# Performance work log

Hardware: AMD Instinct MI355X
Metric: run time of the kernel (lower is better)

The kernel has to match this reference:

```python
import jax, jax.numpy as jnp
import numpy as np

EPS = 1e-6

def _layernorm(x, gamma, beta):
    mu = jnp.mean(x, axis=-1, keepdims=True)
    var = jnp.mean(jnp.square(x - mu), axis=-1, keepdims=True)
    return (x - mu) * jax.lax.rsqrt(var + EPS) * gamma + beta


def setup_inputs() -> dict:
    key = jax.random.key(0)
    ks = jax.random.split(key, 8)
    B, N, C, F = 2, 2048, 1024, 4096
    s = 0.02
    return {
        "x": jax.random.normal(ks[0], (B, N, C), jnp.float32),
        "Wq": jax.random.normal(ks[1], (C, C), jnp.float32) * s,
        "Wk": jax.random.normal(ks[2], (C, C), jnp.float32) * s,
        "Wv": jax.random.normal(ks[3], (C, C), jnp.float32) * s,
        "Wp": jax.random.normal(ks[4], (C, C), jnp.float32) * s,
        "bp": jnp.zeros((C,), jnp.float32),
        "W1": jax.random.normal(ks[5], (C, F), jnp.float32) * s,
        "b1": jnp.zeros((F,), jnp.float32),
        "W2": jax.random.normal(ks[6], (F, C), jnp.float32) * s,
        "b2": jnp.zeros((C,), jnp.float32),
        "gamma1": jnp.ones((C,), jnp.float32),
        "beta1": jnp.zeros((C,), jnp.float32),
        "gamma2": jnp.ones((C,), jnp.float32),
        "beta2": jnp.zeros((C,), jnp.float32),
    }


def reference(x, Wq, Wk, Wv, Wp, bp, W1, b1, W2, b2, gamma1, beta1, gamma2, beta2):
    B, N, C = x.shape
    H = 16
    D = C // H
    scale = D ** -0.5

    xn = _layernorm(x, gamma1, beta1)
    # QKV projections (no bias); q pre-scaled by head_dim**-0.5 as in source
    q = (xn @ Wq * scale).reshape(B, N, H, D).transpose(0, 2, 1, 3)  # bhnd
    k = (xn @ Wk).reshape(B, N, H, D).transpose(0, 2, 1, 3)
    v = (xn @ Wv).reshape(B, N, H, D).transpose(0, 2, 1, 3)

    attn = jax.nn.softmax(jnp.einsum("bhnd,bhmd->bhnm", q, k), axis=-1)
    y = jnp.einsum("bhnm,bhmd->bhnd", attn, v)
    y = y.transpose(0, 2, 1, 3).reshape(B, N, C)
    x = x + (y @ Wp + bp)

    xn2 = _layernorm(x, gamma2, beta2)
    h = jax.nn.gelu(xn2 @ W1 + b1, approximate=False)  # keras 'gelu' is exact
    x = x + (h @ W2 + b2)
    return x
```

## Files before the change

kernel.cpp:

```cpp
#include <hip/hip_runtime.h>
#include <math.h>

#define BN  4096
#define SEQ 2048
#define CH  1024
#define FF  4096
#define NH  16
#define HD  64

typedef short bf16x8 __attribute__((ext_vector_type(8)));
typedef float f32x4  __attribute__((ext_vector_type(4)));

#define MFMA16(a,b,c) __builtin_amdgcn_mfma_f32_16x16x32_bf16(a,b,c,0,0,0)

__device__ __forceinline__ unsigned short f2b(float f){
  unsigned u = __float_as_uint(f);
  u += 0x7fffu + ((u>>16)&1u);
  return (unsigned short)(u>>16);
}

__device__ __forceinline__ unsigned pk2(float a, float b){
  return __builtin_amdgcn_perm(__float_as_uint(b), __float_as_uint(a), 0x07060302u);
}

#if __has_builtin(__builtin_amdgcn_exp2f)
__device__ __forceinline__ float fexp2(float x){ return __builtin_amdgcn_exp2f(x); }
#else
__device__ __forceinline__ float fexp2(float x){
  float r; asm("v_exp_f32 %0, %1" : "=v"(r) : "v"(x)); return r;
}
#endif

__device__ __forceinline__ void gl2lds16(const void* g, void* l){
  __builtin_amdgcn_global_load_lds(
      (__attribute__((address_space(1))) void*)g,
      (__attribute__((address_space(3))) void*)l, 16, 0, 0);
}

__device__ __forceinline__ unsigned xcd_chunk(unsigned id, unsigned nwg){
  const unsigned cpx = nwg >> 3;
  return (id & 7u)*cpx + (id >> 3);
}

__global__ __launch_bounds__(256) void transpose_cvt(const float* __restrict__ in,
    unsigned short* __restrict__ out, int R, int S, float scale)
{
  __shared__ float tile[64][65];
  const int tid = threadIdx.x;
  const int tx = tid & 63, ty = tid >> 6;
  const int s0 = blockIdx.x * 64, r0 = blockIdx.y * 64;
  #pragma unroll
  for (int j = 0; j < 16; j++){
    int r = ty + j*4;
    tile[r][tx] = in[(size_t)(r0 + r)*S + s0 + tx];
  }
  __syncthreads();
  #pragma unroll
  for (int j = 0; j < 16; j++){
    int s = ty + j*4;
    out[(size_t)(s0 + s)*R + r0 + tx] = f2b(tile[tx][s] * scale);
  }
}

__global__ __launch_bounds__(256) void ln_kernel(const float* __restrict__ x,
    const float* __restrict__ gamma, const float* __restrict__ beta,
    unsigned short* __restrict__ out)
{
  const int row = blockIdx.x, tid = threadIdx.x;
  const float4 xv = ((const float4*)(x + (size_t)row*CH))[tid];
  float s  = xv.x + xv.y + xv.z + xv.w;
  float ss = xv.x*xv.x + xv.y*xv.y + xv.z*xv.z + xv.w*xv.w;
  #pragma unroll
  for (int off = 1; off < 64; off <<= 1){
    s  += __shfl_xor(s,  off, 64);
    ss += __shfl_xor(ss, off, 64);
  }
  __shared__ float red[8];
  const int w = tid >> 6;
  if ((tid & 63) == 0){ red[w] = s; red[4+w] = ss; }
  __syncthreads();
  s  = red[0]+red[1]+red[2]+red[3];
  ss = red[4]+red[5]+red[6]+red[7];
  const float mu   = s * (1.f/CH);
  const float rstd = rsqrtf(ss*(1.f/CH) - mu*mu + 1e-6f);
  const float4 g = ((const float4*)gamma)[tid];
  const float4 b = ((const float4*)beta )[tid];
  ushort4 o;
  o.x = f2b((xv.x-mu)*rstd*g.x + b.x);
  o.y = f2b((xv.y-mu)*rstd*g.y + b.y);
  o.z = f2b((xv.z-mu)*rstd*g.z + b.z);
  o.w = f2b((xv.w-mu)*rstd*g.w + b.w);
  ((ushort4*)(out + (size_t)row*CH))[tid] = o;
}

template<int BNT,int BIAS,int GELU,int RES,int OMODE,int SPLITK>
__global__ __launch_bounds__(256,2) void gemm_bt(const unsigned short* __restrict__ A,
    const unsigned short* __restrict__ Bt, const float* __restrict__ bias,
    const float* __restrict__ resid, float* __restrict__ outF,
    unsigned short* __restrict__ outB, unsigned short* __restrict__ outK,
    unsigned short* __restrict__ outV, int M, int Nn, int K)
{
  constexpr int MI  = (BNT==128) ? 4 : 2;
  constexpr int BCH = (BNT==128) ? 4 : 2;
  constexpr int ABYTES = 128*64*2;
  constexpr int BBYTES = BNT*64*2;
  __shared__ __align__(16) char lds[2*ABYTES + 2*BBYTES];
  const int tid = threadIdx.x;
  const int w = tid >> 6, lane = tid & 63;
  const int quad = lane >> 4, l16 = lane & 15;
  const unsigned Wid = xcd_chunk(blockIdx.y*gridDim.x + blockIdx.x,
                                 gridDim.x*gridDim.y);
  const int bx = Wid % gridDim.x, by = Wid / gridDim.x;
  const int m0 = by*128, n0 = bx*BNT;
  const int wm = (BNT==128) ? (w >> 1)*64 : w*32;
  const int wn = (BNT==128) ? (w & 1)*64 : 0;
  const int srow = lane >> 3, sslot = lane & 7;
  f32x4 acc[MI][4] = {};
  const int kseg = SPLITK > 1 ? K / SPLITK : K;
  const int kBeg = SPLITK > 1 ? blockIdx.z * kseg : 0;
  const int nsteps = kseg >> 6;

  auto STAGE = [&](int buf, int k0){
    char* Ad = lds + buf*ABYTES;
    char* Bd = lds + 2*ABYTES + buf*BBYTES;
    #pragma unroll
    for (int i = 0; i < 4; i++){
      const int rb = (w*4 + i)*8;
      const int r = rb + srow;
      const int c = sslot ^ (r & 7);
      gl2lds16(A + (size_t)(m0 + r)*K + k0 + c*8, Ad + rb*128);
    }
    #pragma unroll
    for (int i = 0; i < BCH; i++){
      const int rb = (w*BCH + i)*8;
      const int r = rb + srow;
      const int c = sslot ^ (r & 7);
      gl2lds16(Bt + (size_t)(n0 + r)*K + k0 + c*8, Bd + rb*128);
    }
  };

  STAGE(0, kBeg);
  __syncthreads();
  for (int t = 0; t < nsteps; t++){
    const int cur = t & 1;
    if (t + 1 < nsteps) STAGE(cur ^ 1, kBeg + (t+1)*64);
    const unsigned short* Ac = (const unsigned short*)(lds + cur*ABYTES);
    const unsigned short* Bc = (const unsigned short*)(lds + 2*ABYTES + cur*BBYTES);
    #pragma unroll
    for (int kc = 0; kc < 2; kc++){
      bf16x8 af[MI], bfr[4];
      #pragma unroll
      for (int mi = 0; mi < MI; mi++){
        const int r = wm + mi*16 + l16;
        af[mi] = *(const bf16x8*)(Ac + r*64 + (((kc*4 + quad) ^ (r & 7))*8));
      }
      #pragma unroll
      for (int nj = 0; nj < 4; nj++){
        const int r = wn + nj*16 + l16;
        bfr[nj] = *(const bf16x8*)(Bc + r*64 + (((kc*4 + quad) ^ (r & 7))*8));
      }
      #pragma unroll
      for (int mi = 0; mi < MI; mi++)
        #pragma unroll
        for (int nj = 0; nj < 4; nj++)
          acc[mi][nj] = MFMA16(af[mi], bfr[nj], acc[mi][nj]);
    }
    __syncthreads();
  }

  if (OMODE == 1 || OMODE == 3){
    unsigned short* scr = (unsigned short*)lds + w*(64*64);
    #pragma unroll
    for (int nj = 0; nj < 4; nj++){
      const int col = n0 + wn + nj*16 + l16;
      const float bv = BIAS ? bias[col] : 0.f;
      #pragma unroll
      for (int mi = 0; mi < MI; mi++){
        #pragma unroll
        for (int r = 0; r < 4; r++){
          const int rl = mi*16 + quad*4 + r;
          float v = acc[mi][nj][r] + bv;
          if (GELU) v = 0.5f*v*(1.f + erff(v*0.70710678118654752f));
          if (RES)  v += resid[(size_t)(m0 + wm + rl)*Nn + col];
          const unsigned short b16 = f2b(v);
          if (OMODE == 3 && (n0 + wn) >= 2048){
            const int d = nj*16 + l16;
            scr[d*64 + (((rl & 15) << 2) | (rl >> 4))] = b16;
          } else {
            scr[rl*64 + nj*16 + l16] = b16;
          }
        }
      }
    }
    const int row0 = m0 + wm;
    const int colb = n0 + wn;
    const int sl = (lane & 7)*8;
    #pragma unroll
    for (int j = 0; j < 8; j++){
      const int rr = j*8 + (lane >> 3);
      const bf16x8 vv = *(const bf16x8*)(scr + rr*64 + sl);
      if (OMODE == 1){
        *(bf16x8*)(outB + (size_t)(row0 + rr)*Nn + colb + sl) = vv;
      } else {
        const int cg = colb >> 10;
        if (cg == 0)
          *(bf16x8*)(outB + (size_t)(row0 + rr)*CH + (colb & (CH-1)) + sl) = vv;
        else if (cg == 1)
          *(bf16x8*)(outK + (size_t)(row0 + rr)*CH + (colb & (CH-1)) + sl) = vv;
        else {
          const int bb = row0 >> 11;
          const int hh = (colb & (CH-1)) >> 6;
          *(bf16x8*)(outV + ((size_t)((bb*NH + hh)*HD) + rr)*SEQ + (row0 & (SEQ-1)) + sl) = vv;
        }
      }
    }
    return;
  }
  #pragma unroll
  for (int nj = 0; nj < 4; nj++){
    const int col = n0 + wn + nj*16 + l16;
    const float bv = BIAS ? bias[col] : 0.f;
    #pragma unroll
    for (int mi = 0; mi < MI; mi++){
      #pragma unroll
      for (int r = 0; r < 4; r++){
        const int row = m0 + wm + mi*16 + quad*4 + r;
        float v = acc[mi][nj][r];
        if (SPLITK > 1){
          if (blockIdx.z == 0){
            if (BIAS) v += bias[col];
            if (RES)  v += resid[(size_t)row*Nn + col];
          }
          atomicAdd(&outF[(size_t)row*Nn + col], v);
          continue;
        }
        v += bv;
        if (GELU) v = 0.5f*v*(1.f + erff(v*0.70710678118654752f));
        if (RES)  v += resid[(size_t)row*Nn + col];
        outF[(size_t)row*Nn + col] = v;
      }
    }
  }
}

__global__ __launch_bounds__(256,2) void attn_kernel(const unsigned short* __restrict__ q,
    const unsigned short* __restrict__ k, const unsigned short* __restrict__ vt,
    unsigned short* __restrict__ y)
{
  __shared__ __align__(16) unsigned short Kl[2][64*64];
  __shared__ __align__(16) unsigned short Vl[2][64*64];
  __shared__ __align__(16) unsigned short Pp[4][64*68];
  const int tid = threadIdx.x;
  const int w = tid >> 6, lane = tid & 63;
  const int wq = w & 1, wk = w >> 1;
  const int quad = lane >> 4, l16 = lane & 15;
  const unsigned Wid = xcd_chunk(blockIdx.y*gridDim.x + blockIdx.x,
                                 gridDim.x*gridDim.y);
  const int qt = Wid & 15, bh = Wid >> 4;
  const int b = bh >> 4, h = bh & 15;
  const size_t tb  = ((size_t)b*SEQ)*CH + h*HD;
  const size_t vb_ = (size_t)bh*HD*SEQ;
  const int qr0 = qt*128 + wq*64;

  bf16x8 qf[4][2];
  #pragma unroll
  for (int mi = 0; mi < 4; mi++)
    #pragma unroll
    for (int kc = 0; kc < 2; kc++)
      qf[mi][kc] = *(const bf16x8*)(q + tb + (size_t)(qr0 + mi*16 + l16)*CH + kc*32 + quad*8);

  float sacc[4][4];
  f32x4 o[4][4] = {};
  #pragma unroll
  for (int mi = 0; mi < 4; mi++)
    #pragma unroll
    for (int r = 0; r < 4; r++) sacc[mi][r] = 0.f;

  for (int t = 0; t < 16; t++){
    const int kv0 = wk*1024 + t*64;
    __syncthreads();
    #pragma unroll
    for (int i = 0; i < 8; i++){
      const int r = i*8 + (lane >> 3);
      const int c = (lane & 7) ^ (r & 7);
      if (wq == 0)
        gl2lds16(k  + tb  + (size_t)(kv0 + r)*CH + c*8, (char*)&Kl[wk][0] + i*1024);
      else
        gl2lds16(vt + vb_ + (size_t)r*SEQ + kv0 + c*8, (char*)&Vl[wk][0] + i*1024);
    }
    __syncthreads();

    f32x4 s[4][4] = {};
    #pragma unroll
    for (int kc = 0; kc < 2; kc++){
      #pragma unroll
      for (int nj = 0; nj < 4; nj++){
        bf16x8 kf = *(const bf16x8*)(&Kl[wk][0] + (nj*16 + l16)*64 + (((kc*4 + quad) ^ (l16 & 7))*8));
        #pragma unroll
        for (int mi = 0; mi < 4; mi++)
          s[mi][nj] = MFMA16(qf[mi][kc], kf, s[mi][nj]);
      }
    }
    #pragma unroll
    for (int mi = 0; mi < 4; mi++){
      #pragma unroll
      for (int r = 0; r < 4; r++){
        const float p0 = fexp2(s[mi][0][r]);
        const float p1 = fexp2(s[mi][1][r]);
        const float p2 = fexp2(s[mi][2][r]);
        const float p3 = fexp2(s[mi][3][r]);
        sacc[mi][r] += (p0 + p1) + (p2 + p3);
        uint2 pk;
        pk.x = pk2(p0, p1);
        pk.y = pk2(p2, p3);
        const int prow = mi*16 + quad*4 + r;
        *(uint2*)(&Pp[w][prow*68 + l16*4]) = pk;
      }
    }
    #pragma unroll
    for (int kc = 0; kc < 2; kc++){
      bf16x8 pa[4];
      #pragma unroll
      for (int mi = 0; mi < 4; mi++)
        pa[mi] = *(const bf16x8*)(&Pp[w][(mi*16 + l16)*68 + kc*32 + quad*8]);
      #pragma unroll
      for (int nd = 0; nd < 4; nd++){
        bf16x8 vf = *(const bf16x8*)(&Vl[wk][0] + (nd*16 + l16)*64 + (((kc*4 + quad) ^ (l16 & 7))*8));
        #pragma unroll
        for (int mi = 0; mi < 4; mi++)
          o[mi][nd] = MFMA16(pa[mi], vf, o[mi][nd]);
      }
    }
  }

  __syncthreads();
  float* ob = wq ? (float*)&Vl[0][0] : (float*)&Kl[0][0];
  float* sb = (float*)&Pp[2 + wq][0];
  if (wk == 1){
    #pragma unroll
    for (int mi = 0; mi < 4; mi++)
      #pragma unroll
      for (int nd = 0; nd < 4; nd++)
        #pragma unroll
        for (int r = 0; r < 4; r++){
          const int idx = (mi*4 + nd)*4 + r;
          ob[lane*64 + ((idx + lane) & 63)] = o[mi][nd][r];
        }
    #pragma unroll
    for (int mi = 0; mi < 4; mi++)
      #pragma unroll
      for (int r = 0; r < 4; r++)
        sb[lane*16 + ((mi*4 + r + lane) & 15)] = sacc[mi][r];
  }
  __syncthreads();
  if (wk == 0){
    #pragma unroll
    for (int mi = 0; mi < 4; mi++)
      #pragma unroll
      for (int nd = 0; nd < 4; nd++)
        #pragma unroll
        for (int r = 0; r < 4; r++){
          const int idx = (mi*4 + nd)*4 + r;
          o[mi][nd][r] += ob[lane*64 + ((idx + lane) & 63)];
        }
    #pragma unroll
    for (int mi = 0; mi < 4; mi++){
      #pragma unroll
      for (int r = 0; r < 4; r++){
        float sum = sacc[mi][r] + sb[lane*16 + ((mi*4 + r + lane) & 15)];
        #pragma unroll
        for (int off = 1; off < 16; off <<= 1) sum += __shfl_xor(sum, off, 64);
        const float inv = 1.f / sum;
        const int qr = qr0 + mi*16 + quad*4 + r;
        #pragma unroll
        for (int nd = 0; nd < 4; nd++)
          y[tb + (size_t)qr*CH + nd*16 + l16] = f2b(o[mi][nd][r]*inv);
      }
    }
  }
}

extern "C" void kernel_launch(void* const* d_in, const int* in_sizes, int n_in,
                              void* d_out, int out_size, void* d_ws, size_t ws_size,
                              hipStream_t stream)
{
  (void)in_sizes; (void)n_in; (void)out_size; (void)ws_size;
  const float* x   = (const float*)d_in[0];
  const float* Wq  = (const float*)d_in[1];
  const float* Wk  = (const float*)d_in[2];
  const float* Wv  = (const float*)d_in[3];
  const float* Wp  = (const float*)d_in[4];
  const float* bp  = (const float*)d_in[5];
  const float* W1  = (const float*)d_in[6];
  const float* b1  = (const float*)d_in[7];
  const float* W2  = (const float*)d_in[8];
  const float* b2  = (const float*)d_in[9];
  const float* g1  = (const float*)d_in[10];
  const float* be1 = (const float*)d_in[11];
  const float* g2  = (const float*)d_in[12];
  const float* be2 = (const float*)d_in[13];
  float* out = (float*)d_out;
  char* ws = (char*)d_ws;
  const size_t MB = 1024*1024;
  unsigned short* wq_t = (unsigned short*)(ws +  0*MB);
  unsigned short* wk_t = (unsigned short*)(ws +  2*MB);
  unsigned short* wv_t = (unsigned short*)(ws +  4*MB);
  unsigned short* wp_t = (unsigned short*)(ws +  6*MB);
  unsigned short* w1_t = (unsigned short*)(ws +  8*MB);
  unsigned short* w2_t = (unsigned short*)(ws + 16*MB);
  unsigned short* xn   = (unsigned short*)(ws + 24*MB);
  unsigned short* qb   = (unsigned short*)(ws + 32*MB);
  unsigned short* kb   = (unsigned short*)(ws + 40*MB);
  unsigned short* vtb  = (unsigned short*)(ws + 48*MB);
  unsigned short* yb   = (unsigned short*)(ws + 56*MB);
  float*          x2   = (float*)         (ws + 64*MB);
  unsigned short* xn2  = (unsigned short*)(ws + 80*MB);
  unsigned short* hb   = (unsigned short*)(ws + 88*MB);

  transpose_cvt<<<dim3(16,16),256,0,stream>>>(Wq, wq_t, CH, CH, 0.18033688011112042f);
  transpose_cvt<<<dim3(16,16),256,0,stream>>>(Wk, wk_t, CH, CH, 1.f);
  transpose_cvt<<<dim3(16,16),256,0,stream>>>(Wv, wv_t, CH, CH, 1.f);
  transpose_cvt<<<dim3(16,16),256,0,stream>>>(Wp, wp_t, CH, CH, 1.f);
  transpose_cvt<<<dim3(64,16),256,0,stream>>>(W1, w1_t, CH, FF, 1.f);
  transpose_cvt<<<dim3(16,64),256,0,stream>>>(W2, w2_t, FF, CH, 1.f);

  ln_kernel<<<BN,256,0,stream>>>(x, g1, be1, xn);
  gemm_bt<128,0,0,0,3,0><<<dim3(24,32),256,0,stream>>>(xn, wq_t, nullptr, nullptr,
      nullptr, qb, kb, vtb, BN, 3072, CH);
  attn_kernel<<<dim3(16,32),256,0,stream>>>(qb, kb, vtb, yb);
  gemm_bt<64,1,0,1,0,0><<<dim3(16,32),256,0,stream>>>(yb, wp_t, bp, x, x2,
      nullptr, nullptr, nullptr, BN, CH, CH);
  ln_kernel<<<BN,256,0,stream>>>(x2, g2, be2, xn2);
  gemm_bt<128,1,1,0,1,0><<<dim3(32,32),256,0,stream>>>(xn2, w1_t, b1, nullptr, nullptr,
      hb, nullptr, nullptr, BN, FF, CH);
  gemm_bt<64,1,0,1,0,0><<<dim3(16,32),256,0,stream>>>(hb, w2_t, b2, x2, out,
      nullptr, nullptr, nullptr, BN, CH, FF);
}
```

Measured before the change: 363.0 us.

## Add 256x256-tile 512-thread GEMM for QKV, FFN1, and split-K FFN2

Adds a new gemm256 kernel with 256x256 output tiles, 8 waves, a double-buffered 128KB LDS staging area, and setprio/sched_barrier hints around the MFMA blocks. It is used for the fused QKV projection, the GELU FFN up-projection, and the FFN down-projection. The down-projection uses 4-way split-K with atomic adds into an output zeroed by memset. The aim is more operand reuse per block and fewer blocks. The cost is much larger LDS and register use per block, lower occupancy, and nondeterministic atomic accumulation. The bf16 epilogue path is removed from the old gemm_bt kernel.

```diff
diff --git a/kernel.cpp b/kernel.cpp
--- a/kernel.cpp
+++ b/kernel.cpp
@@ -91,6 +91,154 @@
   o.z = f2b((xv.z-mu)*rstd*g.z + b.z);
   o.w = f2b((xv.w-mu)*rstd*g.w + b.w);
   ((ushort4*)(out + (size_t)row*CH))[tid] = o;
+}
+
+template<int BIAS,int GELU,int RES,int OMODE,int SPLITK>
+__global__ __launch_bounds__(512,2) void gemm256(const unsigned short* __restrict__ A,
+    const unsigned short* __restrict__ Bt, const float* __restrict__ bias,
+    const float* __restrict__ resid, float* __restrict__ outF,
+    unsigned short* __restrict__ outB, unsigned short* __restrict__ outK,
+    unsigned short* __restrict__ outV, int M, int Nn, int K)
+{
+  __shared__ __align__(16) char lds[131072];
+  const int tid = threadIdx.x;
+  const int w = tid >> 6, lane = tid & 63;
+  const int quad = lane >> 4, l16 = lane & 15;
+  const unsigned Wid = xcd_chunk(blockIdx.y*gridDim.x + blockIdx.x,
+                                 gridDim.x*gridDim.y);
+  const int bx = Wid % gridDim.x, by = Wid / gridDim.x;
+  const int m0 = by*256, n0 = bx*256;
+  const int wm = (w >> 2)*128, wn = (w & 3)*64;
+  const int srow = lane >> 3, sslot = lane & 7;
+  f32x4 acc[8][4] = {};
+  const int kseg = SPLITK > 1 ? K / SPLITK : K;
+  const int kBeg = SPLITK > 1 ? blockIdx.z * kseg : 0;
+  const int nt = kseg >> 6;
+
+  auto STAGE = [&](int buf, int k0){
+    char* Ad = lds + buf*32768;
+    char* Bd = lds + 65536 + buf*32768;
+    #pragma unroll
+    for (int i = 0; i < 4; i++){
+      const int ci = w*4 + i;
+      const int r = ci*8 + srow;
+      const int c = sslot ^ srow;
+      gl2lds16(A  + (size_t)(m0 + r)*K + k0 + c*8, Ad + ci*1024);
+      gl2lds16(Bt + (size_t)(n0 + r)*K + k0 + c*8, Bd + ci*1024);
+    }
+  };
+
+  STAGE(0, kBeg);
+  __syncthreads();
+  for (int kt = 0; kt < nt; kt++){
+    const int cur = kt & 1;
+    if (kt + 1 < nt) STAGE(cur ^ 1, kBeg + (kt+1)*64);
+    const unsigned short* Ac = (const unsigned short*)(lds + cur*32768);
+    const unsigned short* Bc = (const unsigned short*)(lds + 65536 + cur*32768);
+    #pragma unroll
+    for (int h = 0; h < 2; h++){
+      bf16x8 af[8], bf[4];
+      #pragma unroll
+      for (int mf = 0; mf < 8; mf++){
+        const int r = wm + mf*16 + l16;
+        af[mf] = *(const bf16x8*)(Ac + r*64 + (((h*4 + quad) ^ (r & 7))*8));
+      }
+      #pragma unroll
+      for (int nf = 0; nf < 4; nf++){
+        const int r = wn + nf*16 + l16;
+        bf[nf] = *(const bf16x8*)(Bc + r*64 + (((h*4 + quad) ^ (r & 7))*8));
+      }
+      __builtin_amdgcn_s_setprio(1);
+      #pragma unroll
+      for (int mf = 0; mf < 8; mf++)
+        #pragma unroll
+        for (int nf = 0; nf < 4; nf++)
+          acc[mf][nf] = MFMA16(af[mf], bf[nf], acc[mf][nf]);
+      __builtin_amdgcn_s_setprio(0);
+      if (h == 0) __builtin_amdgcn_sched_barrier(0);
+    }
+    __syncthreads();
+  }
+
+  const int colb = n0 + wn;
+  const int row0 = m0 + wm;
+  if (OMODE == 1 || OMODE == 3){
+    unsigned short* scr = (unsigned short*)lds + w*8192;
+    const int cg = (OMODE == 3) ? (colb >> 10) : 0;
+    #pragma unroll
+    for (int nf = 0; nf < 4; nf++){
+      const int col = colb + nf*16 + l16;
+      const float bv = BIAS ? bias[col] : 0.f;
+      #pragma unroll
+      for (int mf = 0; mf < 8; mf++){
+        #pragma unroll
+        for (int r = 0; r < 4; r++){
+          const int rl = mf*16 + quad*4 + r;
+          float v = acc[mf][nf][r] + bv;
+          if (GELU) v = 0.5f*v*(1.f + erff(v*0.70710678118654752f));
+          if (RES)  v += resid[(size_t)(row0 + rl)*Nn + col];
+          const unsigned short b16 = f2b(v);
+          if (OMODE == 3 && cg == 2){
+            const int dl = nf*16 + l16;
+            scr[dl*128 + (rl & ~63) + (((rl & 15) << 2) | ((rl >> 4) & 3))] = b16;
+          } else {
+            scr[rl*64 + nf*16 + l16] = b16;
+          }
+        }
+      }
+    }
+    if (OMODE == 3 && cg == 2){
+      const int bb = row0 >> 11;
+      const int hh = (colb & (CH-1)) >> 6;
+      #pragma unroll
+      for (int j = 0; j < 16; j++){
+        const int dl = j*4 + quad;
+        const int t8 = l16*8;
+        const bf16x8 vv = *(const bf16x8*)(scr + dl*128 + t8);
+        *(bf16x8*)(outV + ((size_t)((bb*NH + hh)*HD) + dl)*SEQ
+                        + (row0 & (SEQ-1)) + t8) = vv;
+      }
+    } else {
+      const int sl = (lane & 7)*8;
+      #pragma unroll
+      for (int j = 0; j < 16; j++){
+        const int rr = j*8 + (lane >> 3);
+        const bf16x8 vv = *(const bf16x8*)(scr + rr*64 + sl);
+        if (OMODE == 1)
+          *(bf16x8*)(outB + (size_t)(row0 + rr)*Nn + colb + sl) = vv;
+        else if (cg == 0)
+          *(bf16x8*)(outB + (size_t)(row0 + rr)*CH + (colb & (CH-1)) + sl) = vv;
+        else
+          *(bf16x8*)(outK + (size_t)(row0 + rr)*CH + (colb & (CH-1)) + sl) = vv;
+      }
+    }
+    return;
+  }
+  #pragma unroll
+  for (int nf = 0; nf < 4; nf++){
+    const int col = colb + nf*16 + l16;
+    const float bv = BIAS ? bias[col] : 0.f;
+    #pragma unroll
+    for (int mf = 0; mf < 8; mf++){
+      #pragma unroll
+      for (int r = 0; r < 4; r++){
+        const int row = row0 + mf*16 + quad*4 + r;
+        float v = acc[mf][nf][r];
+        if (SPLITK > 1){
+          if (blockIdx.z == 0){
+            if (BIAS) v += bias[col];
+            if (RES)  v += resid[(size_t)row*Nn + col];
+          }
+          atomicAdd(&outF[(size_t)row*Nn + col], v);
+          continue;
+        }
+        v += bv;
+        if (GELU) v = 0.5f*v*(1.f + erff(v*0.70710678118654752f));
+        if (RES)  v += resid[(size_t)row*Nn + col];
+        outF[(size_t)row*Nn + col] = v;
+      }
+    }
+  }
 }
 
 template<int BNT,int BIAS,int GELU,int RES,int OMODE,int SPLITK>
@@ -168,54 +316,6 @@
     __syncthreads();
   }
 
-  if (OMODE == 1 || OMODE == 3){
-    unsigned short* scr = (unsigned short*)lds + w*(64*64);
-    #pragma unroll
-    for (int nj = 0; nj < 4; nj++){
-      const int col = n0 + wn + nj*16 + l16;
-      const float bv = BIAS ? bias[col] : 0.f;
-      #pragma unroll
-      for (int mi = 0; mi < MI; mi++){
-        #pragma unroll
-        for (int r = 0; r < 4; r++){
-          const int rl = mi*16 + quad*4 + r;
-          float v = acc[mi][nj][r] + bv;
-          if (GELU) v = 0.5f*v*(1.f + erff(v*0.70710678118654752f));
-          if (RES)  v += resid[(size_t)(m0 + wm + rl)*Nn + col];
-          const unsigned short b16 = f2b(v);
-          if (OMODE == 3 && (n0 + wn) >= 2048){
-            const int d = nj*16 + l16;
-            scr[d*64 + (((rl & 15) << 2) | (rl >> 4))] = b16;
-          } else {
-            scr[rl*64 + nj*16 + l16] = b16;
-          }
-        }
-      }
-    }
-    const int row0 = m0 + wm;
-    const int colb = n0 + wn;
-    const int sl = (lane & 7)*8;
-    #pragma unroll
-    for (int j = 0; j < 8; j++){
-      const int rr = j*8 + (lane >> 3);
-      const bf16x8 vv = *(const bf16x8*)(scr + rr*64 + sl);
-      if (OMODE == 1){
-        *(bf16x8*)(outB + (size_t)(row0 + rr)*Nn + colb + sl) = vv;
-      } else {
-        const int cg = colb >> 10;
-        if (cg == 0)
-          *(bf16x8*)(outB + (size_t)(row0 + rr)*CH + (colb & (CH-1)) + sl) = vv;
-        else if (cg == 1)
-          *(bf16x8*)(outK + (size_t)(row0 + rr)*CH + (colb & (CH-1)) + sl) = vv;
-        else {
-          const int bb = row0 >> 11;
-          const int hh = (colb & (CH-1)) >> 6;
-          *(bf16x8*)(outV + ((size_t)((bb*NH + hh)*HD) + rr)*SEQ + (row0 & (SEQ-1)) + sl) = vv;
-        }
-      }
-    }
-    return;
-  }
   #pragma unroll
   for (int nj = 0; nj < 4; nj++){
     const int col = n0 + wn + nj*16 + l16;
@@ -237,7 +337,8 @@
         v += bv;
         if (GELU) v = 0.5f*v*(1.f + erff(v*0.70710678118654752f));
         if (RES)  v += resid[(size_t)row*Nn + col];
-        outF[(size_t)row*Nn + col] = v;
+        if (OMODE == 0) outF[(size_t)row*Nn + col] = v;
+        else outB[(size_t)row*Nn + col] = f2b(v);
       }
     }
   }
@@ -425,14 +526,15 @@
   transpose_cvt<<<dim3(16,64),256,0,stream>>>(W2, w2_t, FF, CH, 1.f);
 
   ln_kernel<<<BN,256,0,stream>>>(x, g1, be1, xn);
-  gemm_bt<128,0,0,0,3,0><<<dim3(24,32),256,0,stream>>>(xn, wq_t, nullptr, nullptr,
+  gemm256<0,0,0,3,0><<<dim3(12,16),512,0,stream>>>(xn, wq_t, nullptr, nullptr,
       nullptr, qb, kb, vtb, BN, 3072, CH);
   attn_kernel<<<dim3(16,32),256,0,stream>>>(qb, kb, vtb, yb);
   gemm_bt<64,1,0,1,0,0><<<dim3(16,32),256,0,stream>>>(yb, wp_t, bp, x, x2,
       nullptr, nullptr, nullptr, BN, CH, CH);
   ln_kernel<<<BN,256,0,stream>>>(x2, g2, be2, xn2);
-  gemm_bt<128,1,1,0,1,0><<<dim3(32,32),256,0,stream>>>(xn2, w1_t, b1, nullptr, nullptr,
+  gemm256<1,1,0,1,0><<<dim3(16,16),512,0,stream>>>(xn2, w1_t, b1, nullptr, nullptr,
       hb, nullptr, nullptr, BN, FF, CH);
-  gemm_bt<64,1,0,1,0,0><<<dim3(16,32),256,0,stream>>>(hb, w2_t, b2, x2, out,
+  hipMemsetAsync(out, 0, (size_t)BN*CH*sizeof(float), stream);
+  gemm256<1,0,1,0,4><<<dim3(4,16,4),512,0,stream>>>(hb, w2_t, b2, x2, out,
       nullptr, nullptr, nullptr, BN, CH, FF);
 }
```

After: 409.5 us. +12.8%, slower.

## Rewrite GEMM mainloop as triple-buffered K=32 pipeline with explicit vmcnt waits

Applied to the files above, without the earlier changes.

Replaces the double-buffered 64-wide K-step GEMM loop with a three-stage ring of 32-wide K tiles. Global-to-LDS pointers are precomputed and advanced incrementally, and a new swizzle is used. Partial s_waitcnt vmcnt plus raw s_barrier let loads two stages ahead stay in flight while MFMAs run. Launch bounds rise to 4 blocks per CU to raise occupancy. The trade-off is that each K tile carries half as many MFMAs per barrier, and the hand-written waitcnt counts must exactly match the issued loads for the result to stay correct.

```diff
diff --git a/kernel.cpp b/kernel.cpp
--- a/kernel.cpp
+++ b/kernel.cpp
@@ -93,18 +93,18 @@
   ((ushort4*)(out + (size_t)row*CH))[tid] = o;
 }
 
-template<int BNT,int BIAS,int GELU,int RES,int OMODE,int SPLITK>
-__global__ __launch_bounds__(256,2) void gemm_bt(const unsigned short* __restrict__ A,
+template<int BNT,int BIAS,int GELU,int RES,int OMODE>
+__global__ __launch_bounds__(256,4) void gemm_p(const unsigned short* __restrict__ A,
     const unsigned short* __restrict__ Bt, const float* __restrict__ bias,
     const float* __restrict__ resid, float* __restrict__ outF,
     unsigned short* __restrict__ outB, unsigned short* __restrict__ outK,
     unsigned short* __restrict__ outV, int M, int Nn, int K)
 {
-  constexpr int MI  = (BNT==128) ? 4 : 2;
-  constexpr int BCH = (BNT==128) ? 4 : 2;
-  constexpr int ABYTES = 128*64*2;
-  constexpr int BBYTES = BNT*64*2;
-  __shared__ __align__(16) char lds[2*ABYTES + 2*BBYTES];
+  constexpr int MI   = (BNT==128) ? 4 : 2;
+  constexpr int ABUF = 8192;
+  constexpr int BBUF = BNT*64;
+  constexpr int BUFB = ABUF + BBUF;
+  __shared__ __align__(16) char lds[3*BUFB];
   const int tid = threadIdx.x;
   const int w = tid >> 6, lane = tid & 63;
   const int quad = lane >> 4, l16 = lane & 15;
@@ -114,65 +114,83 @@
   const int m0 = by*128, n0 = bx*BNT;
   const int wm = (BNT==128) ? (w >> 1)*64 : w*32;
   const int wn = (BNT==128) ? (w & 1)*64 : 0;
-  const int srow = lane >> 3, sslot = lane & 7;
   f32x4 acc[MI][4] = {};
-  const int kseg = SPLITK > 1 ? K / SPLITK : K;
-  const int kBeg = SPLITK > 1 ? blockIdx.z * kseg : 0;
-  const int nsteps = kseg >> 6;
-
-  auto STAGE = [&](int buf, int k0){
-    char* Ad = lds + buf*ABYTES;
-    char* Bd = lds + 2*ABYTES + buf*BBYTES;
-    #pragma unroll
-    for (int i = 0; i < 4; i++){
-      const int rb = (w*4 + i)*8;
-      const int r = rb + srow;
-      const int c = sslot ^ (r & 7);
-      gl2lds16(A + (size_t)(m0 + r)*K + k0 + c*8, Ad + rb*128);
-    }
-    #pragma unroll
-    for (int i = 0; i < BCH; i++){
-      const int rb = (w*BCH + i)*8;
-      const int r = rb + srow;
-      const int c = sslot ^ (r & 7);
-      gl2lds16(Bt + (size_t)(n0 + r)*K + k0 + c*8, Bd + rb*128);
-    }
+  const int nt = K >> 5;
+
+  const int ci0 = w*2, ci1 = w*2 + 1;
+  const int ra0 = ci0*16 + (lane >> 2);
+  const int ra1 = ra0 + 16;
+  const int ga0 = (lane & 3) ^ ((ra0 >> 1) & 3);
+  const int ga1 = (lane & 3) ^ ((ra1 >> 1) & 3);
+  const unsigned short* aS0 = A + (size_t)(m0 + ra0)*K + ga0*8;
+  const unsigned short* aS1 = A + (size_t)(m0 + ra1)*K + ga1*8;
+  const int rb0 = (BNT==128) ? ra0 : (w*16 + (lane >> 2));
+  const int gb0 = (lane & 3) ^ ((rb0 >> 1) & 3);
+  const unsigned short* bS0 = Bt + (size_t)(n0 + rb0)*K + gb0*8;
+  const unsigned short* bS1 = Bt + (size_t)(n0 + ra1)*K + ga1*8;
+
+  auto STAGE = [&](int buf){
+    char* Ad = lds + buf*BUFB;
+    char* Bd = Ad + ABUF;
+    gl2lds16(aS0, Ad + ci0*1024);
+    gl2lds16(aS1, Ad + ci1*1024);
+    if (BNT == 128){
+      gl2lds16(bS0, Bd + ci0*1024);
+      gl2lds16(bS1, Bd + ci1*1024);
+    } else {
+      gl2lds16(bS0, Bd + w*1024);
+    }
+    aS0 += 32; aS1 += 32; bS0 += 32; bS1 += 32;
   };
 
-  STAGE(0, kBeg);
-  __syncthreads();
-  for (int t = 0; t < nsteps; t++){
-    const int cur = t & 1;
-    if (t + 1 < nsteps) STAGE(cur ^ 1, kBeg + (t+1)*64);
-    const unsigned short* Ac = (const unsigned short*)(lds + cur*ABYTES);
-    const unsigned short* Bc = (const unsigned short*)(lds + 2*ABYTES + cur*BBYTES);
-    #pragma unroll
-    for (int kc = 0; kc < 2; kc++){
-      bf16x8 af[MI], bfr[4];
-      #pragma unroll
-      for (int mi = 0; mi < MI; mi++){
-        const int r = wm + mi*16 + l16;
-        af[mi] = *(const bf16x8*)(Ac + r*64 + (((kc*4 + quad) ^ (r & 7))*8));
-      }
-      #pragma unroll
-      for (int nj = 0; nj < 4; nj++){
-        const int r = wn + nj*16 + l16;
-        bfr[nj] = *(const bf16x8*)(Bc + r*64 + (((kc*4 + quad) ^ (r & 7))*8));
-      }
-      #pragma unroll
-      for (int mi = 0; mi < MI; mi++)
-        #pragma unroll
-        for (int nj = 0; nj < 4; nj++)
-          acc[mi][nj] = MFMA16(af[mi], bfr[nj], acc[mi][nj]);
-    }
-    __syncthreads();
-  }
-
+  STAGE(0); STAGE(1);
+  if (BNT == 128) asm volatile("s_waitcnt vmcnt(4)" ::: "memory");
+  else            asm volatile("s_waitcnt vmcnt(3)" ::: "memory");
+  __builtin_amdgcn_s_barrier();
+  __builtin_amdgcn_sched_barrier(0);
+
+  int bufR = 0, bufW = 2;
+  for (int t = 0; t < nt; t++){
+    const bool more = (t + 2 < nt);
+    if (more){ STAGE(bufW); bufW = (bufW == 2) ? 0 : bufW + 1; }
+    const unsigned short* Ac = (const unsigned short*)(lds + bufR*BUFB);
+    const unsigned short* Bc = (const unsigned short*)(lds + bufR*BUFB + ABUF);
+    bf16x8 af[MI], bfr[4];
+    #pragma unroll
+    for (int mi = 0; mi < MI; mi++){
+      const int r = wm + mi*16 + l16;
+      af[mi] = *(const bf16x8*)(Ac + r*32 + ((quad ^ ((r >> 1) & 3))*8));
+    }
+    #pragma unroll
+    for (int nj = 0; nj < 4; nj++){
+      const int r = wn + nj*16 + l16;
+      bfr[nj] = *(const bf16x8*)(Bc + r*32 + ((quad ^ ((r >> 1) & 3))*8));
+    }
+    #pragma unroll
+    for (int mi = 0; mi < MI; mi++)
+      #pragma unroll
+      for (int nj = 0; nj < 4; nj++)
+        acc[mi][nj] = MFMA16(af[mi], bfr[nj], acc[mi][nj]);
+    __builtin_amdgcn_sched_barrier(0);
+    if (more){
+      if (BNT == 128) asm volatile("s_waitcnt vmcnt(4)" ::: "memory");
+      else            asm volatile("s_waitcnt vmcnt(3)" ::: "memory");
+    } else {
+      asm volatile("s_waitcnt vmcnt(0)" ::: "memory");
+    }
+    __builtin_amdgcn_s_barrier();
+    __builtin_amdgcn_sched_barrier(0);
+    bufR = (bufR == 2) ? 0 : bufR + 1;
+  }
+
+  const int colb = n0 + wn;
+  const int row0 = m0 + wm;
   if (OMODE == 1 || OMODE == 3){
-    unsigned short* scr = (unsigned short*)lds + w*(64*64);
+    unsigned short* scr = (unsigned short*)lds + w*4096;
+    const int cg = (OMODE == 3) ? (colb >> 10) : 0;
     #pragma unroll
     for (int nj = 0; nj < 4; nj++){
-      const int col = n0 + wn + nj*16 + l16;
+      const int col = colb + nj*16 + l16;
       const float bv = BIAS ? bias[col] : 0.f;
       #pragma unroll
       for (int mi = 0; mi < MI; mi++){
@@ -181,9 +199,9 @@
           const int rl = mi*16 + quad*4 + r;
           float v = acc[mi][nj][r] + bv;
           if (GELU) v = 0.5f*v*(1.f + erff(v*0.70710678118654752f));
-          if (RES)  v += resid[(size_t)(m0 + wm + rl)*Nn + col];
+          if (RES)  v += resid[(size_t)(row0 + rl)*Nn + col];
           const unsigned short b16 = f2b(v);
-          if (OMODE == 3 && (n0 + wn) >= 2048){
+          if (OMODE == 3 && cg == 2){
             const int d = nj*16 + l16;
             scr[d*64 + (((rl & 15) << 2) | (rl >> 4))] = b16;
           } else {
@@ -192,8 +210,6 @@
         }
       }
     }
-    const int row0 = m0 + wm;
-    const int colb = n0 + wn;
     const int sl = (lane & 7)*8;
     #pragma unroll
     for (int j = 0; j < 8; j++){
@@ -202,7 +218,6 @@
       if (OMODE == 1){
         *(bf16x8*)(outB + (size_t)(row0 + rr)*Nn + colb + sl) = vv;
       } else {
-        const int cg = colb >> 10;
         if (cg == 0)
           *(bf16x8*)(outB + (size_t)(row0 + rr)*CH + (colb & (CH-1)) + sl) = vv;
         else if (cg == 1)
@@ -210,7 +225,8 @@
         else {
           const int bb = row0 >> 11;
           const int hh = (colb & (CH-1)) >> 6;
-          *(bf16x8*)(outV + ((size_t)((bb*NH + hh)*HD) + rr)*SEQ + (row0 & (SEQ-1)) + sl) = vv;
+          *(bf16x8*)(outV + ((size_t)((bb*NH + hh)*HD) + rr)*SEQ
+                          + (row0 & (SEQ-1)) + sl) = vv;
         }
       }
     }
@@ -218,23 +234,14 @@
   }
   #pragma unroll
   for (int nj = 0; nj < 4; nj++){
-    const int col = n0 + wn + nj*16 + l16;
+    const int col = colb + nj*16 + l16;
     const float bv = BIAS ? bias[col] : 0.f;
     #pragma unroll
     for (int mi = 0; mi < MI; mi++){
       #pragma unroll
       for (int r = 0; r < 4; r++){
-        const int row = m0 + wm + mi*16 + quad*4 + r;
-        float v = acc[mi][nj][r];
-        if (SPLITK > 1){
-          if (blockIdx.z == 0){
-            if (BIAS) v += bias[col];
-            if (RES)  v += resid[(size_t)row*Nn + col];
-          }
-          atomicAdd(&outF[(size_t)row*Nn + col], v);
-          continue;
-        }
-        v += bv;
+        const int row = row0 + mi*16 + quad*4 + r;
+        float v = acc[mi][nj][r] + bv;
         if (GELU) v = 0.5f*v*(1.f + erff(v*0.70710678118654752f));
         if (RES)  v += resid[(size_t)row*Nn + col];
         outF[(size_t)row*Nn + col] = v;
@@ -425,14 +432,14 @@
   transpose_cvt<<<dim3(16,64),256,0,stream>>>(W2, w2_t, FF, CH, 1.f);
 
   ln_kernel<<<BN,256,0,stream>>>(x, g1, be1, xn);
-  gemm_bt<128,0,0,0,3,0><<<dim3(24,32),256,0,stream>>>(xn, wq_t, nullptr, nullptr,
+  gemm_p<128,0,0,0,3><<<dim3(24,32),256,0,stream>>>(xn, wq_t, nullptr, nullptr,
       nullptr, qb, kb, vtb, BN, 3072, CH);
   attn_kernel<<<dim3(16,32),256,0,stream>>>(qb, kb, vtb, yb);
-  gemm_bt<64,1,0,1,0,0><<<dim3(16,32),256,0,stream>>>(yb, wp_t, bp, x, x2,
+  gemm_p<64,1,0,1,0><<<dim3(16,32),256,0,stream>>>(yb, wp_t, bp, x, x2,
       nullptr, nullptr, nullptr, BN, CH, CH);
   ln_kernel<<<BN,256,0,stream>>>(x2, g2, be2, xn2);
-  gemm_bt<128,1,1,0,1,0><<<dim3(32,32),256,0,stream>>>(xn2, w1_t, b1, nullptr, nullptr,
+  gemm_p<128,1,1,0,1><<<dim3(32,32),256,0,stream>>>(xn2, w1_t, b1, nullptr, nullptr,
       hb, nullptr, nullptr, BN, FF, CH);
-  gemm_bt<64,1,0,1,0,0><<<dim3(16,32),256,0,stream>>>(hb, w2_t, b2, x2, out,
+  gemm_p<64,1,0,1,0><<<dim3(16,32),256,0,stream>>>(hb, w2_t, b2, x2, out,
       nullptr, nullptr, nullptr, BN, CH, FF);
 }
```

Measured after the change: 353.3 us. 2.7% less time.
